# Kernel tuning notes

Measured on AMD Instinct MI355X. Metric: run time of the kernel, lower is better.

## Reference

```python
import jax, jax.numpy as jnp
import numpy as np

UNITS = 1024
D_Q = 1024
D_V = 1024


def setup_inputs() -> dict:
    key = jax.random.key(0)
    ks = jax.random.split(key, 8)
    B, S = 32, 2048
    query = jax.random.normal(ks[0], (B, D_Q), dtype=jnp.float32)
    values = jax.random.normal(ks[1], (B, S, D_V), dtype=jnp.float32)
    # Keras Dense params (glorot-ish scale for weights, zero bias init kept random-free)
    W1 = jax.random.normal(ks[2], (D_V, UNITS), dtype=jnp.float32) / np.sqrt(D_V)
    b1 = jnp.zeros((UNITS,), dtype=jnp.float32)
    W2 = jax.random.normal(ks[3], (D_Q, UNITS), dtype=jnp.float32) / np.sqrt(D_Q)
    b2 = jnp.zeros((UNITS,), dtype=jnp.float32)
    V = jax.random.normal(ks[4], (UNITS, 1), dtype=jnp.float32) / np.sqrt(UNITS)
    bV = jnp.zeros((1,), dtype=jnp.float32)
    return {"query": query, "values": values, "W1": W1, "b1": b1,
            "W2": W2, "b2": b2, "V": V, "bV": bV}


def reference(query, values, W1, b1, W2, b2, V, bV):
    # query: [B, d_q], values: [B, S, d_v]
    proj_v = jnp.einsum('bsd,du->bsu', values, W1) + b1        # [B, S, U]
    proj_q = (query @ W2 + b2)[:, None, :]                      # [B, 1, U]
    score = jnp.tanh(proj_v + proj_q) @ V + bV                  # [B, S, 1]
    attention_weights = jax.nn.softmax(score, axis=1)           # [B, S, 1]
    context_vector = jnp.sum(attention_weights * values, axis=1)  # [B, d_v]
    return (context_vector, attention_weights)
```

## Files before the change

kernel.cpp:

```cpp
#include <hip/hip_runtime.h>
#include <math.h>

#define B_  32
#define S_  2048
#define DV  1024
#define U_  1024

typedef __attribute__((ext_vector_type(8))) short bf16x8;
typedef __attribute__((ext_vector_type(4))) float f32x4;

__device__ inline unsigned short f2bf(float f) {
    unsigned int x = __float_as_uint(f);
    return (unsigned short)((x + 0x7fffu + ((x >> 16) & 1u)) >> 16);
}

__device__ inline float tanh_fast(float x) {
    float ax = fabsf(x);
    float e  = __expf(ax + ax);
    float t  = 1.0f - __fdividef(2.0f, e + 1.0f);
    return copysignf(t, x);
}

__global__ void init_kernel(const float* __restrict__ b1, const float* __restrict__ b2,
                            float* __restrict__ t, float* __restrict__ ctx,
                            float* __restrict__ scores) {
    int i = blockIdx.x * 256 + threadIdx.x;
    scores[i] = 0.f;
    if (i < B_ * U_) {
        int u = i & (U_ - 1);
        t[i]   = b1[u] + b2[u];
        ctx[i] = 0.f;
    }
}

__global__ void projq_kernel(const float* __restrict__ q, const float* __restrict__ W2,
                             float* __restrict__ t) {
    int b  = blockIdx.x;
    int ks = blockIdx.y;
    int tid = threadIdx.x;
    __shared__ float qs[256];
    qs[tid] = q[b * DV + ks * 256 + tid];
    __syncthreads();
    float a0 = 0.f, a1 = 0.f, a2 = 0.f, a3 = 0.f;
    const float* w = W2 + (size_t)(ks * 256) * U_;
    for (int d = 0; d < 256; ++d) {
        float qd = qs[d];
        const float* wr = w + (size_t)d * U_ + tid;
        a0 += qd * wr[0];
        a1 += qd * wr[256];
        a2 += qd * wr[512];
        a3 += qd * wr[768];
    }
    atomicAdd(&t[b * U_ + tid      ], a0);
    atomicAdd(&t[b * U_ + tid + 256], a1);
    atomicAdd(&t[b * U_ + tid + 512], a2);
    atomicAdd(&t[b * U_ + tid + 768], a3);
}

__global__ void cvt_values(const float* __restrict__ v, unsigned short* __restrict__ o) {
    size_t i = ((size_t)blockIdx.x * 256 + threadIdx.x) * 8;
    float4 f0 = *(const float4*)(v + i);
    float4 f1 = *(const float4*)(v + i + 4);
    union { unsigned short s[8]; uint4 u; } p;
    p.s[0] = f2bf(f0.x); p.s[1] = f2bf(f0.y); p.s[2] = f2bf(f0.z); p.s[3] = f2bf(f0.w);
    p.s[4] = f2bf(f1.x); p.s[5] = f2bf(f1.y); p.s[6] = f2bf(f1.z); p.s[7] = f2bf(f1.w);
    *(uint4*)(o + i) = p.u;
}

__global__ void prep_w1t(const float* __restrict__ W1, unsigned short* __restrict__ W1T) {
    __shared__ float tile[64][65];
    int k0 = blockIdx.x * 64, u0 = blockIdx.y * 64;
    int t = threadIdx.x;
    int lr = t >> 4, lc = (t & 15) * 4;
#pragma unroll
    for (int i = 0; i < 4; ++i) {
        float4 f = *(const float4*)&W1[(size_t)(k0 + lr + i * 16) * U_ + u0 + lc];
        tile[lr + i * 16][lc + 0] = f.x; tile[lr + i * 16][lc + 1] = f.y;
        tile[lr + i * 16][lc + 2] = f.z; tile[lr + i * 16][lc + 3] = f.w;
    }
    __syncthreads();
    int ur = t >> 2, kq = (t & 3) * 16;
    union { unsigned short s[8]; uint4 u; } p0, p1;
#pragma unroll
    for (int e = 0; e < 8; ++e) p0.s[e] = f2bf(tile[kq + e][ur]);
#pragma unroll
    for (int e = 0; e < 8; ++e) p1.s[e] = f2bf(tile[kq + 8 + e][ur]);
    unsigned short* dst = W1T + (size_t)(u0 + ur) * 1024 + k0 + kq;
    *(uint4*)dst       = p0.u;
    *(uint4*)(dst + 8) = p1.u;
}

template<bool ABF16>
__launch_bounds__(256, 2)
__global__ void scores_mfma(const void* __restrict__ aPtr,
                            const unsigned short* __restrict__ W1T,
                            const float* __restrict__ t,
                            const float* __restrict__ V,
                            float* __restrict__ scores) {
    __shared__ unsigned short sA[128 * 40];
    __shared__ unsigned short sB[256 * 40];
    __shared__ float fscore[128];

    const int tid  = threadIdx.x;
    const int lane = tid & 63;
    const int wave = tid >> 6;
    const int wm = wave & 1, wn = wave >> 1;
    const int l15 = lane & 15, lq = lane >> 4;

    const int id    = blockIdx.x;
    const int utile = (id >> 3) & 3;
    const int stile = (id & 7) | ((id >> 5) << 3);
    const size_t row0 = (size_t)stile * 128;
    const int b       = (int)(row0 >> 11);
    const int s_local = (int)(row0 & 2047);
    const int u0      = utile * 256;

    if (tid < 128) fscore[tid] = 0.f;

    const int ar = tid >> 1, ak = (tid & 1) << 4;
    const int br = tid >> 1, bk = (tid & 1) << 4;

    const float* Af = (const float*)aPtr + (row0 + ar) * 1024 + ak;
    const unsigned short* Ab = (const unsigned short*)aPtr + (row0 + ar) * 1024 + ak;
    const unsigned short* Bp0 = W1T + (size_t)(u0 + br) * 1024 + bk;
    const unsigned short* Bp1 = Bp0 + 128 * 1024;

    f32x4 acc[4][8];
#pragma unroll
    for (int i = 0; i < 4; ++i)
#pragma unroll
        for (int j = 0; j < 8; ++j) acc[i][j] = (f32x4)0.f;

    uint4 sa0, sa1, sb0, sb1, sb2, sb3;
    float4 fa0, fa1, fa2, fa3;

    if (ABF16) {
        sa0 = *(const uint4*)(Ab);
        sa1 = *(const uint4*)(Ab + 8);
    } else {
        fa0 = *(const float4*)(Af);
        fa1 = *(const float4*)(Af + 4);
        fa2 = *(const float4*)(Af + 8);
        fa3 = *(const float4*)(Af + 12);
    }
    sb0 = *(const uint4*)(Bp0);
    sb1 = *(const uint4*)(Bp0 + 8);
    sb2 = *(const uint4*)(Bp1);
    sb3 = *(const uint4*)(Bp1 + 8);

    for (int k0 = 0; k0 < 1024; k0 += 32) {
        __syncthreads();
        if (ABF16) {
            *(uint4*)&sA[ar * 40 + ak]     = sa0;
            *(uint4*)&sA[ar * 40 + ak + 8] = sa1;
        } else {
            union { unsigned short s[8]; uint4 u; } p0, p1;
            p0.s[0] = f2bf(fa0.x); p0.s[1] = f2bf(fa0.y); p0.s[2] = f2bf(fa0.z); p0.s[3] = f2bf(fa0.w);
            p0.s[4] = f2bf(fa1.x); p0.s[5] = f2bf(fa1.y); p0.s[6] = f2bf(fa1.z); p0.s[7] = f2bf(fa1.w);
            p1.s[0] = f2bf(fa2.x); p1.s[1] = f2bf(fa2.y); p1.s[2] = f2bf(fa2.z); p1.s[3] = f2bf(fa2.w);
            p1.s[4] = f2bf(fa3.x); p1.s[5] = f2bf(fa3.y); p1.s[6] = f2bf(fa3.z); p1.s[7] = f2bf(fa3.w);
            *(uint4*)&sA[ar * 40 + ak]     = p0.u;
            *(uint4*)&sA[ar * 40 + ak + 8] = p1.u;
        }
        *(uint4*)&sB[br * 40 + bk]           = sb0;
        *(uint4*)&sB[br * 40 + bk + 8]       = sb1;
        *(uint4*)&sB[(br + 128) * 40 + bk]     = sb2;
        *(uint4*)&sB[(br + 128) * 40 + bk + 8] = sb3;

        if (k0 + 32 < 1024) {
            int nk = k0 + 32;
            if (ABF16) {
                sa0 = *(const uint4*)(Ab + nk);
                sa1 = *(const uint4*)(Ab + nk + 8);
            } else {
                fa0 = *(const float4*)(Af + nk);
                fa1 = *(const float4*)(Af + nk + 4);
                fa2 = *(const float4*)(Af + nk + 8);
                fa3 = *(const float4*)(Af + nk + 12);
            }
            sb0 = *(const uint4*)(Bp0 + nk);
            sb1 = *(const uint4*)(Bp0 + nk + 8);
            sb2 = *(const uint4*)(Bp1 + nk);
            sb3 = *(const uint4*)(Bp1 + nk + 8);
        }
        __syncthreads();

        bf16x8 af[4];
#pragma unroll
        for (int i = 0; i < 4; ++i)
            af[i] = *(const bf16x8*)&sA[(64 * wm + 16 * i + l15) * 40 + lq * 8];
#pragma unroll
        for (int j = 0; j < 8; ++j) {
            bf16x8 bfj = *(const bf16x8*)&sB[(128 * wn + 16 * j + l15) * 40 + lq * 8];
#pragma unroll
            for (int i = 0; i < 4; ++i)
                acc[i][j] = __builtin_amdgcn_mfma_f32_16x16x32_bf16(af[i], bfj, acc[i][j], 0, 0, 0);
        }
    }

    float tu[8], vu[8];
#pragma unroll
    for (int j = 0; j < 8; ++j) {
        int u = u0 + 128 * wn + 16 * j + l15;
        tu[j] = t[b * U_ + u];
        vu[j] = V[u];
    }
#pragma unroll
    for (int i = 0; i < 4; ++i) {
#pragma unroll
        for (int r = 0; r < 4; ++r) {
            float p = 0.f;
#pragma unroll
            for (int j = 0; j < 8; ++j) p += tanh_fast(acc[i][j][r] + tu[j]) * vu[j];
            p += __shfl_xor(p, 1);
            p += __shfl_xor(p, 2);
            p += __shfl_xor(p, 4);
            p += __shfl_xor(p, 8);
            if (l15 == 0) atomicAdd(&fscore[64 * wm + 16 * i + lq * 4 + r], p);
        }
    }
    __syncthreads();
    if (tid < 128) atomicAdd(&scores[(size_t)b * S_ + s_local + tid], fscore[tid]);
}

__launch_bounds__(256, 2)
__global__ void scores_vec(const float* __restrict__ values, const float* __restrict__ W1,
                           const float* __restrict__ t, const float* __restrict__ V,
                           float* __restrict__ scores) {
    __shared__ float vA[16][132];
    __shared__ float vB[16][68];
    __shared__ float fscore[128];
    const int b   = blockIdx.y;
    const int s0  = blockIdx.x * 128;
    const int tid = threadIdx.x;
    const int tx  = tid & 15, ty = tid >> 4;
    if (tid < 128) fscore[tid] = 0.f;
    const float* vbase = values + ((size_t)b * S_ + s0) * (size_t)DV;
    const int lm = tid >> 2, lkq = (tid & 3) * 4;
    const int lbk = tid >> 4, lbj = (tid & 15) * 4;
    for (int nt = 0; nt < U_ / 64; ++nt) {
        const int u0 = nt * 64;
        float acc[8][4];
#pragma unroll
        for (int i = 0; i < 8; ++i)
#pragma unroll
            for (int j = 0; j < 4; ++j) acc[i][j] = 0.f;
        for (int k0 = 0; k0 < DV; k0 += 16) {
            __syncthreads();
            const float4 v0 = *(const float4*)(vbase + (size_t)lm * DV + k0 + lkq);
            const float4 v1 = *(const float4*)(vbase + (size_t)(lm + 64) * DV + k0 + lkq);
            vA[lkq + 0][lm] = v0.x; vA[lkq + 1][lm] = v0.y;
            vA[lkq + 2][lm] = v0.z; vA[lkq + 3][lm] = v0.w;
            vA[lkq + 0][lm + 64] = v1.x; vA[lkq + 1][lm + 64] = v1.y;
            vA[lkq + 2][lm + 64] = v1.z; vA[lkq + 3][lm + 64] = v1.w;
            *(float4*)&vB[lbk][lbj] = *(const float4*)(W1 + (size_t)(k0 + lbk) * U_ + u0 + lbj);
            __syncthreads();
#pragma unroll
            for (int k = 0; k < 16; ++k) {
                float4 va0 = *(const float4*)&vA[k][ty * 8];
                float4 va1 = *(const float4*)&vA[k][ty * 8 + 4];
                float4 vb  = *(const float4*)&vB[k][tx * 4];
                float a_[8] = {va0.x, va0.y, va0.z, va0.w, va1.x, va1.y, va1.z, va1.w};
                float b_[4] = {vb.x, vb.y, vb.z, vb.w};
#pragma unroll
                for (int i = 0; i < 8; ++i)
#pragma unroll
                    for (int j = 0; j < 4; ++j) acc[i][j] += a_[i] * b_[j];
            }
        }
        float tq[4], vv[4];
#pragma unroll
        for (int j = 0; j < 4; ++j) {
            int u = u0 + tx * 4 + j;
            tq[j] = t[b * U_ + u];
            vv[j] = V[u];
        }
#pragma unroll
        for (int i = 0; i < 8; ++i) {
            float p = 0.f;
#pragma unroll
            for (int j = 0; j < 4; ++j) p += tanhf(acc[i][j] + tq[j]) * vv[j];
            p += __shfl_down(p, 8, 16);
            p += __shfl_down(p, 4, 16);
            p += __shfl_down(p, 2, 16);
            p += __shfl_down(p, 1, 16);
            if (tx == 0) fscore[ty * 8 + i] += p;
        }
    }
    __syncthreads();
    if (tid < 128) scores[(size_t)b * S_ + s0 + tid] = fscore[tid];
}

__global__ void softmax_kernel(const float* __restrict__ scores, float* __restrict__ wout) {
    int b = blockIdx.x;
    int tid = threadIdx.x;
    __shared__ float red[256];
    float v[8];
    float m = -1e30f;
#pragma unroll
    for (int i = 0; i < 8; ++i) {
        v[i] = scores[(size_t)b * S_ + tid + i * 256];
        m = fmaxf(m, v[i]);
    }
    red[tid] = m; __syncthreads();
    for (int off = 128; off > 0; off >>= 1) {
        if (tid < off) red[tid] = fmaxf(red[tid], red[tid + off]);
        __syncthreads();
    }
    m = red[0];
    __syncthreads();
    float s = 0.f;
#pragma unroll
    for (int i = 0; i < 8; ++i) { v[i] = __expf(v[i] - m); s += v[i]; }
    red[tid] = s; __syncthreads();
    for (int off = 128; off > 0; off >>= 1) {
        if (tid < off) red[tid] += red[tid + off];
        __syncthreads();
    }
    float inv = 1.f / red[0];
#pragma unroll
    for (int i = 0; i < 8; ++i) wout[(size_t)b * S_ + tid + i * 256] = v[i] * inv;
}

__global__ void context_kernel(const float* __restrict__ values, const float* __restrict__ w,
                               float* __restrict__ ctx) {
    int b  = blockIdx.x;
    int dc = blockIdx.y;
    int sc = blockIdx.z;
    int tid = threadIdx.x;
    int d = dc * 256 + tid;
    __shared__ float ws_[256];
    ws_[tid] = w[(size_t)b * S_ + sc * 256 + tid];
    __syncthreads();
    float acc = 0.f;
    const float* vp = values + ((size_t)b * S_ + sc * 256) * (size_t)DV + d;
#pragma unroll 4
    for (int s = 0; s < 256; ++s) acc += ws_[s] * vp[(size_t)s * DV];
    atomicAdd(&ctx[b * DV + d], acc);
}

extern "C" void kernel_launch(void* const* d_in, const int* in_sizes, int n_in,
                              void* d_out, int out_size, void* d_ws, size_t ws_size,
                              hipStream_t stream) {
    const float* query  = (const float*)d_in[0];
    const float* values = (const float*)d_in[1];
    const float* W1     = (const float*)d_in[2];
    const float* b1     = (const float*)d_in[3];
    const float* W2     = (const float*)d_in[4];
    const float* b2     = (const float*)d_in[5];
    const float* V      = (const float*)d_in[6];

    float* out  = (float*)d_out;
    float* ctx  = out;
    float* wout = out + B_ * DV;

    char* ws = (char*)d_ws;
    const size_t W1T_BYTES = (size_t)U_ * DV * 2;
    const size_t T_BYTES   = (size_t)B_ * U_ * 4;
    const size_t SC_BYTES  = (size_t)B_ * S_ * 4;
    const size_t ABF_BYTES = (size_t)B_ * S_ * DV * 2;

    if (ws_size >= W1T_BYTES + T_BYTES + SC_BYTES + ABF_BYTES) {
        unsigned short* W1T = (unsigned short*)ws;
        float* t      = (float*)(ws + W1T_BYTES);
        float* scores = t + B_ * U_;
        unsigned short* Abf = (unsigned short*)(scores + B_ * S_);

        init_kernel   <<<dim3(256),      256, 0, stream>>>(b1, b2, t, ctx, scores);
        projq_kernel  <<<dim3(32, 4),    256, 0, stream>>>(query, W2, t);
        cvt_values    <<<dim3(32768),    256, 0, stream>>>(values, Abf);
        prep_w1t      <<<dim3(16, 16),   256, 0, stream>>>(W1, W1T);
        scores_mfma<true><<<dim3(2048),  256, 0, stream>>>(Abf, W1T, t, V, scores);
        softmax_kernel<<<dim3(32),       256, 0, stream>>>(scores, wout);
        context_kernel<<<dim3(32, 4, 8), 256, 0, stream>>>(values, wout, ctx);
    } else if (ws_size >= W1T_BYTES + T_BYTES + SC_BYTES) {
        unsigned short* W1T = (unsigned short*)ws;
        float* t      = (float*)(ws + W1T_BYTES);
        float* scores = t + B_ * U_;

        init_kernel   <<<dim3(256),      256, 0, stream>>>(b1, b2, t, ctx, scores);
        projq_kernel  <<<dim3(32, 4),    256, 0, stream>>>(query, W2, t);
        prep_w1t      <<<dim3(16, 16),   256, 0, stream>>>(W1, W1T);
        scores_mfma<false><<<dim3(2048), 256, 0, stream>>>(values, W1T, t, V, scores);
        softmax_kernel<<<dim3(32),       256, 0, stream>>>(scores, wout);
        context_kernel<<<dim3(32, 4, 8), 256, 0, stream>>>(values, wout, ctx);
    } else {
        float* t      = (float*)ws;
        float* scores = t + B_ * U_;

        init_kernel   <<<dim3(256),      256, 0, stream>>>(b1, b2, t, ctx, scores);
        projq_kernel  <<<dim3(32, 4),    256, 0, stream>>>(query, W2, t);
        scores_vec    <<<dim3(16, 32),   256, 0, stream>>>(values, W1, t, V, scores);
        softmax_kernel<<<dim3(32),       256, 0, stream>>>(scores, wout);
        context_kernel<<<dim3(32, 4, 8), 256, 0, stream>>>(values, wout, ctx);
    }
}
```

Before: 631.8 us.

## Add double-buffered direct-to-LDS MFMA scores kernel with swizzled shared layout

Adds a new scores GEMM kernel for the bf16 path. It uses global_load_lds to copy A and W1T tiles straight into LDS, double-buffers the K loop so the next tile's loads overlap the current tile's MFMAs, and XOR-swizzles the LDS layout to avoid bank conflicts. It also reorders block IDs so blocks that share a U tile run close together, and raises wave priority around the MFMA block. The cost is a larger shared-memory footprint and register pressure from a 256x128 tile with 32 accumulators per wave.

```diff
diff --git a/kernel.cpp b/kernel.cpp
--- a/kernel.cpp
+++ b/kernel.cpp
@@ -19,6 +19,13 @@
     float e  = __expf(ax + ax);
     float t  = 1.0f - __fdividef(2.0f, e + 1.0f);
     return copysignf(t, x);
+}
+
+__device__ __forceinline__ void gload16(const void* g, void* l) {
+    __builtin_amdgcn_global_load_lds(
+        (const __attribute__((address_space(1))) void*)g,
+        (__attribute__((address_space(3))) void*)l,
+        16, 0, 0);
 }
 
 __global__ void init_kernel(const float* __restrict__ b1, const float* __restrict__ b2,
@@ -88,6 +95,134 @@
     unsigned short* dst = W1T + (size_t)(u0 + ur) * 1024 + k0 + kq;
     *(uint4*)dst       = p0.u;
     *(uint4*)(dst + 8) = p1.u;
+}
+
+__launch_bounds__(256, 2)
+__global__ void scores_mfma2(const unsigned short* __restrict__ Abf,
+                             const unsigned short* __restrict__ W1T,
+                             const float* __restrict__ tvec,
+                             const float* __restrict__ V,
+                             float* __restrict__ scores) {
+    __shared__ unsigned short sA[2 * 128 * 64];
+    __shared__ unsigned short sB[2 * 64 * 64];
+
+    const int tid  = threadIdx.x;
+    const int lane = tid & 63;
+    const int wave = tid >> 6;
+    const int wm   = wave & 1;
+    const int wn   = wave >> 1;
+    const int l15  = lane & 15;
+    const int lq   = lane >> 4;
+
+    const int id    = blockIdx.x;
+    const int utile = (id >> 3) & 7;
+    const int stile = (id & 7) | ((id >> 6) << 3);
+    const size_t row0 = (size_t)stile * 256;
+    const int b       = (int)(row0 >> 11);
+    const int s_local = (int)(row0 & 2047);
+    const int u0      = utile * 128;
+
+    const unsigned short* aS[4];
+    const unsigned short* bS[2];
+    char* aD[4];
+    char* bD[2];
+#pragma unroll
+    for (int j = 0; j < 4; ++j) {
+        int L = j * 4096 + tid * 16;
+        int line = L >> 7, p = (L >> 4) & 7;
+        int c = p ^ (line & 7);
+        int row = line * 2 + (c >> 2);
+        int kq = c & 3;
+        aS[j] = Abf + (row0 + row) * 1024 + kq * 8;
+        aD[j] = (char*)sA + j * 4096 + wave * 1024;
+    }
+#pragma unroll
+    for (int j = 0; j < 2; ++j) {
+        int L = j * 4096 + tid * 16;
+        int line = L >> 7, p = (L >> 4) & 7;
+        int c = p ^ (line & 7);
+        int row = line * 2 + (c >> 2);
+        int kq = c & 3;
+        bS[j] = W1T + (size_t)(u0 + row) * 1024 + kq * 8;
+        bD[j] = (char*)sB + j * 4096 + wave * 1024;
+    }
+
+    const int prd = ((l15 & 1) * 4 + lq) ^ ((l15 >> 1) & 7);
+    const unsigned short* paBase = sA + (wm * 64 + (l15 >> 1)) * 64 + prd * 8;
+    const unsigned short* pbBase = sB + (wn * 32 + (l15 >> 1)) * 64 + prd * 8;
+
+    f32x4 acc[8][4];
+#pragma unroll
+    for (int m = 0; m < 8; ++m)
+#pragma unroll
+        for (int n = 0; n < 4; ++n) acc[m][n] = (f32x4)0.f;
+
+#pragma unroll
+    for (int j = 0; j < 4; ++j) gload16(aS[j], aD[j]);
+#pragma unroll
+    for (int j = 0; j < 2; ++j) gload16(bS[j], bD[j]);
+#pragma unroll
+    for (int j = 0; j < 4; ++j) aS[j] += 32;
+#pragma unroll
+    for (int j = 0; j < 2; ++j) bS[j] += 32;
+    __syncthreads();
+
+    for (int kt = 0; kt < 32; ++kt) {
+        const int cur = kt & 1;
+        if (kt < 31) {
+            const int nb = cur ^ 1;
+#pragma unroll
+            for (int j = 0; j < 4; ++j) gload16(aS[j], aD[j] + nb * 16384);
+#pragma unroll
+            for (int j = 0; j < 2; ++j) gload16(bS[j], bD[j] + nb * 8192);
+#pragma unroll
+            for (int j = 0; j < 4; ++j) aS[j] += 32;
+#pragma unroll
+            for (int j = 0; j < 2; ++j) bS[j] += 32;
+        }
+        const unsigned short* pa = paBase + cur * 8192;
+        const unsigned short* pb = pbBase + cur * 4096;
+        bf16x8 af[8], bfr[4];
+#pragma unroll
+        for (int m = 0; m < 8; ++m) af[m] = *(const bf16x8*)(pa + m * 512);
+#pragma unroll
+        for (int n = 0; n < 4; ++n) bfr[n] = *(const bf16x8*)(pb + n * 512);
+        __builtin_amdgcn_s_setprio(1);
+#pragma unroll
+        for (int n = 0; n < 4; ++n)
+#pragma unroll
+            for (int m = 0; m < 8; ++m)
+                acc[m][n] = __builtin_amdgcn_mfma_f32_16x16x32_bf16(af[m], bfr[n], acc[m][n], 0, 0, 0);
+        __builtin_amdgcn_s_setprio(0);
+        __syncthreads();
+    }
+
+    float* fscore = (float*)sA;
+    fscore[tid] = 0.f;
+    __syncthreads();
+    float tu[4], vu[4];
+#pragma unroll
+    for (int n = 0; n < 4; ++n) {
+        int u = u0 + wn * 64 + n * 16 + l15;
+        tu[n] = tvec[b * U_ + u];
+        vu[n] = V[u];
+    }
+#pragma unroll
+    for (int m = 0; m < 8; ++m) {
+#pragma unroll
+        for (int r = 0; r < 4; ++r) {
+            float p = 0.f;
+#pragma unroll
+            for (int n = 0; n < 4; ++n) p += tanh_fast(acc[m][n][r] + tu[n]) * vu[n];
+            p += __shfl_xor(p, 1);
+            p += __shfl_xor(p, 2);
+            p += __shfl_xor(p, 4);
+            p += __shfl_xor(p, 8);
+            if (l15 == 0) atomicAdd(&fscore[wm * 128 + m * 16 + lq * 4 + r], p);
+        }
+    }
+    __syncthreads();
+    atomicAdd(&scores[(size_t)b * S_ + s_local + tid], fscore[tid]);
 }
 
 template<bool ABF16>
@@ -370,7 +505,7 @@
         projq_kernel  <<<dim3(32, 4),    256, 0, stream>>>(query, W2, t);
         cvt_values    <<<dim3(32768),    256, 0, stream>>>(values, Abf);
         prep_w1t      <<<dim3(16, 16),   256, 0, stream>>>(W1, W1T);
-        scores_mfma<true><<<dim3(2048),  256, 0, stream>>>(Abf, W1T, t, V, scores);
+        scores_mfma2  <<<dim3(2048),     256, 0, stream>>>(Abf, W1T, t, V, scores);
         softmax_kernel<<<dim3(32),       256, 0, stream>>>(scores, wout);
         context_kernel<<<dim3(32, 4, 8), 256, 0, stream>>>(values, wout, ctx);
     } else if (ws_size >= W1T_BYTES + T_BYTES + SC_BYTES) {
```

Result: slower. 644.9 us (+2.1%).

## Add 8-wave 256x256 MFMA scores kernel with direct-to-LDS async loads

Applied to the files above, without the earlier changes.

Replaces the 4-wave scores GEMM in the main path with a 512-thread kernel computing 256x256 tiles. It stages A and B through global_load_lds into XOR-swizzled LDS and interleaves manual vmcnt waits, barriers and priority raises with MFMA phases so loads overlap compute. It also splits projq across 16 K-chunks to expose more parallelism. In exchange it uses 128KB of LDS per block (about one block per CU), hand-tuned waitcnt sequencing that can fail subtly, and more atomics into the scores buffer.

```diff
diff --git a/kernel.cpp b/kernel.cpp
--- a/kernel.cpp
+++ b/kernel.cpp
@@ -20,6 +20,17 @@
     float t  = 1.0f - __fdividef(2.0f, e + 1.0f);
     return copysignf(t, x);
 }
+
+__device__ __forceinline__ void gload16(const void* g, void* l) {
+    __builtin_amdgcn_global_load_lds(
+        (const __attribute__((address_space(1))) void*)g,
+        (__attribute__((address_space(3))) void*)l,
+        16, 0, 0);
+}
+
+#define ASM_VMCNT(N) asm volatile("s_waitcnt vmcnt(" #N ")" ::: "memory")
+#define ASM_LGKM0()  do { asm volatile("s_waitcnt lgkmcnt(0)" ::: "memory"); \
+                          __builtin_amdgcn_sched_barrier(0); } while (0)
 
 __global__ void init_kernel(const float* __restrict__ b1, const float* __restrict__ b2,
                             float* __restrict__ t, float* __restrict__ ctx,
@@ -38,12 +49,12 @@
     int b  = blockIdx.x;
     int ks = blockIdx.y;
     int tid = threadIdx.x;
-    __shared__ float qs[256];
-    qs[tid] = q[b * DV + ks * 256 + tid];
+    __shared__ float qs[64];
+    if (tid < 64) qs[tid] = q[b * DV + ks * 64 + tid];
     __syncthreads();
     float a0 = 0.f, a1 = 0.f, a2 = 0.f, a3 = 0.f;
-    const float* w = W2 + (size_t)(ks * 256) * U_;
-    for (int d = 0; d < 256; ++d) {
+    const float* w = W2 + (size_t)(ks * 64) * U_;
+    for (int d = 0; d < 64; ++d) {
         float qd = qs[d];
         const float* wr = w + (size_t)d * U_ + tid;
         a0 += qd * wr[0];
@@ -88,6 +99,196 @@
     unsigned short* dst = W1T + (size_t)(u0 + ur) * 1024 + k0 + kq;
     *(uint4*)dst       = p0.u;
     *(uint4*)(dst + 8) = p1.u;
+}
+
+#define MFMA16(MB, NB)                                                          \
+    _Pragma("unroll") for (int ks = 0; ks < 2; ++ks)                            \
+    _Pragma("unroll") for (int n = 0; n < 2; ++n)                               \
+    _Pragma("unroll") for (int m = 0; m < 4; ++m)                               \
+        acc[(MB)+m][(NB)+n] = __builtin_amdgcn_mfma_f32_16x16x32_bf16(          \
+            af[m][ks], bf[n][ks], acc[(MB)+m][(NB)+n], 0, 0, 0);
+
+__launch_bounds__(512, 2)
+__global__ void scores_mfma8(const unsigned short* __restrict__ Abf,
+                             const unsigned short* __restrict__ W1T,
+                             const float* __restrict__ tvec,
+                             const float* __restrict__ V,
+                             float* __restrict__ scores) {
+    __shared__ __align__(16) char lds[131072];
+
+    const int tid  = threadIdx.x;
+    const int lane = tid & 63;
+    const int wave = tid >> 6;
+    const int wm   = wave >> 2;
+    const int wn   = wave & 3;
+    const int l15  = lane & 15;
+    const int lq   = lane >> 4;
+
+    const int id    = blockIdx.x;
+    const int wg    = (id & 7) * 128 + (id >> 3);
+    const int utile = wg & 3;
+    const int stile = wg >> 2;
+    const size_t row0 = (size_t)stile * 256;
+    const int b       = (int)(row0 >> 11);
+    const int s_local = (int)(row0 & 2047);
+    const int u0      = utile * 256;
+
+    const int rowst = wave * 8 + (lane >> 3);
+    const int kch8  = ((lane & 7) ^ ((lane >> 3) & 7)) * 8;
+    const unsigned short* aSrc = Abf + (row0 + rowst) * 1024 + kch8;
+    const unsigned short* bSrc = W1T + (size_t)(u0 + rowst) * 1024 + kch8;
+    char* const dstW = lds + wave * 1024;
+
+    const int ao0 = wm * 16384 + l15 * 128 + ((lq ^ (l15 & 7)) << 4);
+    const int ao1 = ao0 ^ 64;
+    const int bo0 = 32768 + (wn >> 1) * 16384 + (wn & 1) * 8192
+                  + l15 * 128 + ((lq ^ (l15 & 7)) << 4);
+    const int bo1 = bo0 ^ 64;
+
+    f32x4 acc[8][4];
+#pragma unroll
+    for (int m = 0; m < 8; ++m)
+#pragma unroll
+        for (int n = 0; n < 4; ++n) acc[m][n] = (f32x4)0.f;
+
+    bf16x8 af[4][2];
+    bf16x8 bf[2][2];
+
+    auto stage2 = [&](const unsigned short* s, int dOff) {
+        gload16(s,             dstW + dOff);
+        gload16(s + 64 * 1024, dstW + dOff + 8192);
+    };
+    auto readA4 = [&](int base) {
+#pragma unroll
+        for (int m = 0; m < 4; ++m) {
+            af[m][0] = *(const bf16x8*)(lds + base + m * 2048 + ao0);
+            af[m][1] = *(const bf16x8*)(lds + base + m * 2048 + ao1);
+        }
+    };
+    auto readB2 = [&](int base) {
+#pragma unroll
+        for (int n = 0; n < 2; ++n) {
+            bf[n][0] = *(const bf16x8*)(lds + base + n * 2048 + bo0);
+            bf[n][1] = *(const bf16x8*)(lds + base + n * 2048 + bo1);
+        }
+    };
+
+    stage2(aSrc,          0);
+    stage2(aSrc + 131072, 16384);
+    stage2(bSrc,          32768);
+    stage2(bSrc + 131072, 49152);
+    stage2(aSrc + 64,     65536);
+    __builtin_amdgcn_sched_barrier(0);
+    ASM_VMCNT(2);
+    __builtin_amdgcn_s_barrier();
+    __builtin_amdgcn_sched_barrier(0);
+
+    for (int it = 0; it < 8; ++it) {
+        const bool pf = (it < 7);
+        readA4(0);
+        readB2(0);
+        stage2(aSrc + 64 + 131072, 81920);
+        __builtin_amdgcn_s_barrier();
+        ASM_LGKM0();
+        __builtin_amdgcn_s_setprio(1);
+        MFMA16(0, 0);
+        __builtin_amdgcn_s_setprio(0);
+        __builtin_amdgcn_s_barrier();
+        readB2(2 * 2048);
+        stage2(bSrc + 64, 98304);
+        __builtin_amdgcn_s_barrier();
+        ASM_LGKM0();
+        __builtin_amdgcn_s_setprio(1);
+        MFMA16(0, 2);
+        __builtin_amdgcn_s_setprio(0);
+        __builtin_amdgcn_s_barrier();
+        readA4(4 * 2048);
+        stage2(bSrc + 64 + 131072, 114688);
+        __builtin_amdgcn_s_barrier();
+        ASM_LGKM0();
+        __builtin_amdgcn_s_setprio(1);
+        MFMA16(4, 2);
+        __builtin_amdgcn_s_setprio(0);
+        __builtin_amdgcn_s_barrier();
+        readB2(0);
+        if (pf) stage2(aSrc + 128, 0);
+        __builtin_amdgcn_s_barrier();
+        ASM_LGKM0();
+        __builtin_amdgcn_s_setprio(1);
+        MFMA16(4, 0);
+        __builtin_amdgcn_s_setprio(0);
+        __builtin_amdgcn_sched_barrier(0);
+        if (pf) { ASM_VMCNT(2); } else { ASM_VMCNT(0); }
+        __builtin_amdgcn_s_barrier();
+        __builtin_amdgcn_sched_barrier(0);
+        readA4(65536);
+        readB2(65536);
+        if (pf) stage2(aSrc + 128 + 131072, 16384);
+        __builtin_amdgcn_s_barrier();
+        ASM_LGKM0();
+        __builtin_amdgcn_s_setprio(1);
+        MFMA16(0, 0);
+        __builtin_amdgcn_s_setprio(0);
+        __builtin_amdgcn_s_barrier();
+        readB2(65536 + 2 * 2048);
+        if (pf) stage2(bSrc + 128, 32768);
+        __builtin_amdgcn_s_barrier();
+        ASM_LGKM0();
+        __builtin_amdgcn_s_setprio(1);
+        MFMA16(0, 2);
+        __builtin_amdgcn_s_setprio(0);
+        __builtin_amdgcn_s_barrier();
+        readA4(65536 + 4 * 2048);
+        if (pf) stage2(bSrc + 128 + 131072, 49152);
+        __builtin_amdgcn_s_barrier();
+        ASM_LGKM0();
+        __builtin_amdgcn_s_setprio(1);
+        MFMA16(4, 2);
+        __builtin_amdgcn_s_setprio(0);
+        __builtin_amdgcn_s_barrier();
+        readB2(65536);
+        if (pf) stage2(aSrc + 192, 65536);
+        __builtin_amdgcn_s_barrier();
+        ASM_LGKM0();
+        __builtin_amdgcn_s_setprio(1);
+        MFMA16(4, 0);
+        __builtin_amdgcn_s_setprio(0);
+        __builtin_amdgcn_sched_barrier(0);
+        if (pf) { ASM_VMCNT(2); }
+        __builtin_amdgcn_s_barrier();
+        __builtin_amdgcn_sched_barrier(0);
+
+        aSrc += 128;
+        bSrc += 128;
+    }
+
+    __syncthreads();
+    float* fscore = (float*)lds;
+    if (tid < 256) fscore[tid] = 0.f;
+    __syncthreads();
+    float tu[4], vu[4];
+#pragma unroll
+    for (int n = 0; n < 4; ++n) {
+        int u = u0 + wn * 64 + n * 16 + l15;
+        tu[n] = tvec[b * U_ + u];
+        vu[n] = V[u];
+    }
+#pragma unroll
+    for (int m = 0; m < 8; ++m) {
+#pragma unroll
+        for (int r = 0; r < 4; ++r) {
+            float p = 0.f;
+#pragma unroll
+            for (int n = 0; n < 4; ++n) p += tanh_fast(acc[m][n][r] + tu[n]) * vu[n];
+            p += __shfl_xor(p, 1);
+            p += __shfl_xor(p, 2);
+            p += __shfl_xor(p, 4);
+            p += __shfl_xor(p, 8);
+            if (l15 == 0) atomicAdd(&fscore[wm * 128 + m * 16 + lq * 4 + r], p);
+        }
+    }
+    __syncthreads();
+    if (tid < 256) atomicAdd(&scores[(size_t)b * S_ + s_local + tid], fscore[tid]);
 }
 
 template<bool ABF16>
@@ -367,10 +568,10 @@
         unsigned short* Abf = (unsigned short*)(scores + B_ * S_);
 
         init_kernel   <<<dim3(256),      256, 0, stream>>>(b1, b2, t, ctx, scores);
-        projq_kernel  <<<dim3(32, 4),    256, 0, stream>>>(query, W2, t);
+        projq_kernel  <<<dim3(32, 16),   256, 0, stream>>>(query, W2, t);
         cvt_values    <<<dim3(32768),    256, 0, stream>>>(values, Abf);
         prep_w1t      <<<dim3(16, 16),   256, 0, stream>>>(W1, W1T);
-        scores_mfma<true><<<dim3(2048),  256, 0, stream>>>(Abf, W1T, t, V, scores);
+        scores_mfma8  <<<dim3(1024),     512, 0, stream>>>(Abf, W1T, t, V, scores);
         softmax_kernel<<<dim3(32),       256, 0, stream>>>(scores, wout);
         context_kernel<<<dim3(32, 4, 8), 256, 0, stream>>>(values, wout, ctx);
     } else if (ws_size >= W1T_BYTES + T_BYTES + SC_BYTES) {
@@ -379,7 +580,7 @@
         float* scores = t + B_ * U_;
 
         init_kernel   <<<dim3(256),      256, 0, stream>>>(b1, b2, t, ctx, scores);
-        projq_kernel  <<<dim3(32, 4),    256, 0, stream>>>(query, W2, t);
+        projq_kernel  <<<dim3(32, 16),   256, 0, stream>>>(query, W2, t);
         prep_w1t      <<<dim3(16, 16),   256, 0, stream>>>(W1, W1T);
         scores_mfma<false><<<dim3(2048), 256, 0, stream>>>(values, W1T, t, V, scores);
         softmax_kernel<<<dim3(32),       256, 0, stream>>>(scores, wout);
@@ -389,7 +590,7 @@
         float* scores = t + B_ * U_;
 
         init_kernel   <<<dim3(256),      256, 0, stream>>>(b1, b2, t, ctx, scores);
-        projq_kernel  <<<dim3(32, 4),    256, 0, stream>>>(query, W2, t);
+        projq_kernel  <<<dim3(32, 16),   256, 0, stream>>>(query, W2, t);
         scores_vec    <<<dim3(16, 32),   256, 0, stream>>>(values, W1, t, V, scores);
         softmax_kernel<<<dim3(32),       256, 0, stream>>>(scores, wout);
         context_kernel<<<dim3(32, 4, 8), 256, 0, stream>>>(values, wout, ctx);
```

Measured after the change: 597.8 us. 5.4% less time.

## Pre-tile bf16 values into swizzled layout and use direct-to-LDS MFMA scores kernel

Applied to the files above, without the earlier changes.

Replaces the flat fp32-to-bf16 conversion with a kernel that writes values in a pre-tiled, XOR-swizzled layout matching the GEMM's LDS tiles. A new 128x128-tile MFMA scores kernel loads those tiles with global_load_lds straight into shared memory, at occupancy 3 and with a remapped block order for cache locality. The projq kernel is split across more blocks, and the context kernel uses float4 loads with a different split over the sequence. This aims to cut LDS staging overhead and bank conflicts in the dominant GEMM, at the cost of more partial-sum atomics and a single-buffered load/compute loop with two barriers per k-step.

```diff
diff --git a/kernel.cpp b/kernel.cpp
--- a/kernel.cpp
+++ b/kernel.cpp
@@ -12,6 +12,13 @@
 __device__ inline unsigned short f2bf(float f) {
     unsigned int x = __float_as_uint(f);
     return (unsigned short)((x + 0x7fffu + ((x >> 16) & 1u)) >> 16);
+}
+
+__device__ inline uint4 pack8(float4 a, float4 b) {
+    union { unsigned short s[8]; uint4 u; } p;
+    p.s[0] = f2bf(a.x); p.s[1] = f2bf(a.y); p.s[2] = f2bf(a.z); p.s[3] = f2bf(a.w);
+    p.s[4] = f2bf(b.x); p.s[5] = f2bf(b.y); p.s[6] = f2bf(b.z); p.s[7] = f2bf(b.w);
+    return p.u;
 }
 
 __device__ inline float tanh_fast(float x) {
@@ -19,6 +26,13 @@
     float e  = __expf(ax + ax);
     float t  = 1.0f - __fdividef(2.0f, e + 1.0f);
     return copysignf(t, x);
+}
+
+__device__ __forceinline__ void gload16(const void* g, void* l) {
+    __builtin_amdgcn_global_load_lds(
+        (const __attribute__((address_space(1))) void*)g,
+        (__attribute__((address_space(3))) void*)l,
+        16, 0, 0);
 }
 
 __global__ void init_kernel(const float* __restrict__ b1, const float* __restrict__ b2,
@@ -38,12 +52,12 @@
     int b  = blockIdx.x;
     int ks = blockIdx.y;
     int tid = threadIdx.x;
-    __shared__ float qs[256];
-    qs[tid] = q[b * DV + ks * 256 + tid];
+    __shared__ float qs[64];
+    if (tid < 64) qs[tid] = q[b * DV + ks * 64 + tid];
     __syncthreads();
     float a0 = 0.f, a1 = 0.f, a2 = 0.f, a3 = 0.f;
-    const float* w = W2 + (size_t)(ks * 256) * U_;
-    for (int d = 0; d < 256; ++d) {
+    const float* w = W2 + (size_t)(ks * 64) * U_;
+    for (int d = 0; d < 64; ++d) {
         float qd = qs[d];
         const float* wr = w + (size_t)d * U_ + tid;
         a0 += qd * wr[0];
@@ -57,14 +71,34 @@
     atomicAdd(&t[b * U_ + tid + 768], a3);
 }
 
-__global__ void cvt_values(const float* __restrict__ v, unsigned short* __restrict__ o) {
-    size_t i = ((size_t)blockIdx.x * 256 + threadIdx.x) * 8;
-    float4 f0 = *(const float4*)(v + i);
-    float4 f1 = *(const float4*)(v + i + 4);
-    union { unsigned short s[8]; uint4 u; } p;
-    p.s[0] = f2bf(f0.x); p.s[1] = f2bf(f0.y); p.s[2] = f2bf(f0.z); p.s[3] = f2bf(f0.w);
-    p.s[4] = f2bf(f1.x); p.s[5] = f2bf(f1.y); p.s[6] = f2bf(f1.z); p.s[7] = f2bf(f1.w);
-    *(uint4*)(o + i) = p.u;
+__global__ __launch_bounds__(256)
+void cvt_t128(const float* __restrict__ v, char* __restrict__ o) {
+    __shared__ __align__(16) char sm[32 * 1056];
+    const int stile = blockIdx.x;
+    const int g     = blockIdx.y;
+    const int t     = threadIdx.x;
+    const int tl    = t & 127;
+    const int th    = t >> 7;
+    const int kts   = tl >> 2;
+    const int kq    = tl & 3;
+    const int rowg  = stile * 128 + g * 16;
+#pragma unroll
+    for (int p = 0; p < 8; ++p) {
+        int i = p * 2 + th;
+        const float4* src = (const float4*)(v + (size_t)(rowg + i) * 1024 + tl * 8);
+        float4 f0 = src[0], f1 = src[1];
+        int c   = (i & 1) * 4 + kq;
+        int pch = c ^ ((i >> 1) & 7);
+        *(uint4*)(sm + kts * 1056 + (i >> 1) * 128 + pch * 16) = pack8(f0, f1);
+    }
+    __syncthreads();
+#pragma unroll
+    for (int q = 0; q < 8; ++q) {
+        int kt = q * 4 + (t >> 6);
+        uint4 w = *(const uint4*)(sm + kt * 1056 + (t & 63) * 16);
+        *(uint4*)(o + (size_t)stile * 262144 + (size_t)kt * 8192
+                  + g * 1024 + (t & 63) * 16) = w;
+    }
 }
 
 __global__ void prep_w1t(const float* __restrict__ W1, unsigned short* __restrict__ W1T) {
@@ -88,6 +122,107 @@
     unsigned short* dst = W1T + (size_t)(u0 + ur) * 1024 + k0 + kq;
     *(uint4*)dst       = p0.u;
     *(uint4*)(dst + 8) = p1.u;
+}
+
+__launch_bounds__(256, 3)
+__global__ void scores_m97(const char* __restrict__ AbfT,
+                           const unsigned short* __restrict__ W1T,
+                           const float* __restrict__ tvec,
+                           const float* __restrict__ V,
+                           float* __restrict__ scores) {
+    __shared__ __align__(16) char lds[16384];
+
+    const int tid  = threadIdx.x;
+    const int lane = tid & 63;
+    const int wave = tid >> 6;
+    const int wm   = wave >> 1;
+    const int wn   = wave & 1;
+    const int l15  = lane & 15;
+    const int lq   = lane >> 4;
+
+    const int id    = blockIdx.x;
+    const int wg    = (id & 7) * 512 + (id >> 3);
+    const int utile = wg & 7;
+    const int stile = wg >> 3;
+    const size_t row0 = (size_t)stile * 128;
+    const int b       = (int)(row0 >> 11);
+    const int s_local = (int)(row0 & 2047);
+    const int u0      = utile * 128;
+
+    const char* aS0 = AbfT + (size_t)stile * 262144 + tid * 16;
+    const char* aS1 = aS0 + 4096;
+    char* const aD0 = lds + wave * 1024;
+    char* const aD1 = aD0 + 4096;
+    const unsigned short* bS0;
+    const unsigned short* bS1;
+    {
+        int L0 = tid * 16;
+        int ln0 = L0 >> 7, p0 = (L0 >> 4) & 7, c0 = p0 ^ (ln0 & 7);
+        bS0 = W1T + (size_t)(u0 + ln0 * 2 + (c0 >> 2)) * 1024 + (c0 & 3) * 8;
+        int L1 = 4096 + tid * 16;
+        int ln1 = L1 >> 7, p1 = (L1 >> 4) & 7, c1 = p1 ^ (ln1 & 7);
+        bS1 = W1T + (size_t)(u0 + ln1 * 2 + (c1 >> 2)) * 1024 + (c1 & 3) * 8;
+    }
+    char* const bD0 = lds + 8192 + wave * 1024;
+    char* const bD1 = bD0 + 4096;
+
+    const int prd = ((l15 & 1) * 4 + lq) ^ ((l15 >> 1) & 7);
+    const int aOff = (wm * 32 + (l15 >> 1)) * 128 + prd * 16;
+    const int bOff = 8192 + (wn * 32 + (l15 >> 1)) * 128 + prd * 16;
+
+    f32x4 acc[4][4];
+#pragma unroll
+    for (int m = 0; m < 4; ++m)
+#pragma unroll
+        for (int n = 0; n < 4; ++n) acc[m][n] = (f32x4)0.f;
+
+    for (int kt = 0; kt < 32; ++kt) {
+        __syncthreads();
+        gload16(aS0 + (size_t)kt * 8192, aD0);
+        gload16(aS1 + (size_t)kt * 8192, aD1);
+        gload16(bS0 + kt * 32, bD0);
+        gload16(bS1 + kt * 32, bD1);
+        __syncthreads();
+
+        bf16x8 af[4], bf[4];
+#pragma unroll
+        for (int m = 0; m < 4; ++m) af[m] = *(const bf16x8*)(lds + aOff + m * 1024);
+#pragma unroll
+        for (int n = 0; n < 4; ++n) bf[n] = *(const bf16x8*)(lds + bOff + n * 1024);
+#pragma unroll
+        for (int n = 0; n < 4; ++n)
+#pragma unroll
+            for (int m = 0; m < 4; ++m)
+                acc[m][n] = __builtin_amdgcn_mfma_f32_16x16x32_bf16(af[m], bf[n], acc[m][n], 0, 0, 0);
+    }
+
+    __syncthreads();
+    float* fscore = (float*)lds;
+    if (tid < 128) fscore[tid] = 0.f;
+    __syncthreads();
+    float tu[4], vu[4];
+#pragma unroll
+    for (int n = 0; n < 4; ++n) {
+        int u = u0 + wn * 64 + n * 16 + l15;
+        tu[n] = tvec[b * U_ + u];
+        vu[n] = V[u];
+    }
+#pragma unroll
+    for (int m = 0; m < 4; ++m) {
+#pragma unroll
+        for (int r = 0; r < 4; ++r) {
+            float p = 0.f;
+#pragma unroll
+            for (int n = 0; n < 4; ++n) p += tanh_fast(acc[m][n][r] + tu[n]) * vu[n];
+            p += __shfl_xor(p, 1);
+            p += __shfl_xor(p, 2);
+            p += __shfl_xor(p, 4);
+            p += __shfl_xor(p, 8);
+            if (l15 == 0) atomicAdd(&fscore[wm * 64 + m * 16 + lq * 4 + r], p);
+        }
+    }
+    __syncthreads();
+    if (tid < 128) atomicAdd(&scores[(size_t)b * S_ + s_local + tid], fscore[tid]);
 }
 
 template<bool ABF16>
@@ -324,19 +459,23 @@
 
 __global__ void context_kernel(const float* __restrict__ values, const float* __restrict__ w,
                                float* __restrict__ ctx) {
-    int b  = blockIdx.x;
-    int dc = blockIdx.y;
-    int sc = blockIdx.z;
+    int b   = blockIdx.x;
+    int sc  = blockIdx.y;
     int tid = threadIdx.x;
-    int d = dc * 256 + tid;
-    __shared__ float ws_[256];
-    ws_[tid] = w[(size_t)b * S_ + sc * 256 + tid];
-    __syncthreads();
-    float acc = 0.f;
-    const float* vp = values + ((size_t)b * S_ + sc * 256) * (size_t)DV + d;
+    __shared__ float ws_[128];
+    if (tid < 128) ws_[tid] = w[(size_t)b * S_ + sc * 128 + tid];
+    __syncthreads();
+    const float4* vp = (const float4*)(values + ((size_t)b * S_ + sc * 128) * DV) + tid;
+    float ax = 0.f, ay = 0.f, az = 0.f, aw = 0.f;
 #pragma unroll 4
-    for (int s = 0; s < 256; ++s) acc += ws_[s] * vp[(size_t)s * DV];
-    atomicAdd(&ctx[b * DV + d], acc);
+    for (int s = 0; s < 128; ++s) {
+        float4 v = vp[(size_t)s * 256];
+        float wv = ws_[s];
+        ax += wv * v.x; ay += wv * v.y; az += wv * v.z; aw += wv * v.w;
+    }
+    float* c = ctx + b * DV + tid * 4;
+    atomicAdd(c + 0, ax); atomicAdd(c + 1, ay);
+    atomicAdd(c + 2, az); atomicAdd(c + 3, aw);
 }
 
 extern "C" void kernel_launch(void* const* d_in, const int* in_sizes, int n_in,
@@ -364,34 +503,34 @@
         unsigned short* W1T = (unsigned short*)ws;
         float* t      = (float*)(ws + W1T_BYTES);
         float* scores = t + B_ * U_;
-        unsigned short* Abf = (unsigned short*)(scores + B_ * S_);
+        char*  AbfT   = (char*)(scores + B_ * S_);
 
         init_kernel   <<<dim3(256),      256, 0, stream>>>(b1, b2, t, ctx, scores);
-        projq_kernel  <<<dim3(32, 4),    256, 0, stream>>>(query, W2, t);
-        cvt_values    <<<dim3(32768),    256, 0, stream>>>(values, Abf);
+        projq_kernel  <<<dim3(32, 16),   256, 0, stream>>>(query, W2, t);
+        cvt_t128      <<<dim3(512, 8),   256, 0, stream>>>(values, AbfT);
         prep_w1t      <<<dim3(16, 16),   256, 0, stream>>>(W1, W1T);
-        scores_mfma<true><<<dim3(2048),  256, 0, stream>>>(Abf, W1T, t, V, scores);
+        scores_m97    <<<dim3(4096),     256, 0, stream>>>(AbfT, W1T, t, V, scores);
         softmax_kernel<<<dim3(32),       256, 0, stream>>>(scores, wout);
-        context_kernel<<<dim3(32, 4, 8), 256, 0, stream>>>(values, wout, ctx);
+        context_kernel<<<dim3(32, 16),   256, 0, stream>>>(values, wout, ctx);
     } else if (ws_size >= W1T_BYTES + T_BYTES + SC_BYTES) {
         unsigned short* W1T = (unsigned short*)ws;
         float* t      = (float*)(ws + W1T_BYTES);
         float* scores = t + B_ * U_;
 
         init_kernel   <<<dim3(256),      256, 0, stream>>>(b1, b2, t, ctx, scores);
-        projq_kernel  <<<dim3(32, 4),    256, 0, stream>>>(query, W2, t);
+        projq_kernel  <<<dim3(32, 16),   256, 0, stream>>>(query, W2, t);
         prep_w1t      <<<dim3(16, 16),   256, 0, stream>>>(W1, W1T);
         scores_mfma<false><<<dim3(2048), 256, 0, stream>>>(values, W1T, t, V, scores);
         softmax_kernel<<<dim3(32),       256, 0, stream>>>(scores, wout);
-        context_kernel<<<dim3(32, 4, 8), 256, 0, stream>>>(values, wout, ctx);
+        context_kernel<<<dim3(32, 16),   256, 0, stream>>>(values, wout, ctx);
     } else {
         float* t      = (float*)ws;
         float* scores = t + B_ * U_;
 
         init_kernel   <<<dim3(256),      256, 0, stream>>>(b1, b2, t, ctx, scores);
-        projq_kernel  <<<dim3(32, 4),    256, 0, stream>>>(query, W2, t);
+        projq_kernel  <<<dim3(32, 16),   256, 0, stream>>>(query, W2, t);
         scores_vec    <<<dim3(16, 32),   256, 0, stream>>>(values, W1, t, V, scores);
         softmax_kernel<<<dim3(32),       256, 0, stream>>>(scores, wout);
-        context_kernel<<<dim3(32, 4, 8), 256, 0, stream>>>(values, wout, ctx);
-    }
-}
+        context_kernel<<<dim3(32, 16),   256, 0, stream>>>(values, wout, ctx);
+    }
+}
```

Measured after the change: 633.2 us. Within noise of the previous version (+0.2%).
